# Performance work log

Measured on AMD Instinct MI355X. Metric: run time of the kernel, lower is better.

Reference implementation:

```python
import jax, jax.numpy as jnp
import numpy as np

N, K, IN_DIM, OUT_DIM = 100000, 16, 64, 64
BN_EPS = 1e-5


def setup_inputs() -> dict:
    key = jax.random.key(0)
    ks = jax.random.split(key, 12)
    def lin(k, fan_in, shape):
        bound = 1.0 / np.sqrt(fan_in)
        return jax.random.uniform(k, shape, jnp.float32, -bound, bound)
    return {
        'points': jax.random.normal(ks[0], (N, 3), jnp.float32),
        'neighbors': jax.random.randint(ks[1], (N, K), 0, N + 1, jnp.int32),
        'feats': jax.random.normal(ks[2], (N, IN_DIM), jnp.float32),
        'q_w': lin(ks[3], IN_DIM, (OUT_DIM, IN_DIM)), 'q_b': lin(ks[3], IN_DIM, (OUT_DIM,)),
        'k_w': lin(ks[4], IN_DIM, (OUT_DIM, IN_DIM)), 'k_b': lin(ks[4], IN_DIM, (OUT_DIM,)),
        'v_w': lin(ks[5], IN_DIM, (OUT_DIM, IN_DIM)), 'v_b': lin(ks[5], IN_DIM, (OUT_DIM,)),
        'p_w': lin(ks[6], 3, (OUT_DIM, 3)), 'p_b': lin(ks[6], 3, (OUT_DIM,)),
        'p_gamma': jnp.ones((OUT_DIM,), jnp.float32), 'p_beta': jnp.zeros((OUT_DIM,), jnp.float32),
        'w_w': lin(ks[7], OUT_DIM, (OUT_DIM, OUT_DIM)), 'w_b': lin(ks[7], OUT_DIM, (OUT_DIM,)),
        'w_gamma': jnp.ones((OUT_DIM,), jnp.float32), 'w_beta': jnp.zeros((OUT_DIM,), jnp.float32),
    }


def _bn_relu(x, gamma, beta):
    # BatchNorm1d (training mode, biased var) over all axes except channel (last), then ReLU
    mean = jnp.mean(x, axis=(0, 1), keepdims=True)
    var = jnp.mean(jnp.square(x - mean), axis=(0, 1), keepdims=True)
    y = (x - mean) * jax.lax.rsqrt(var + BN_EPS) * gamma + beta
    return jax.nn.relu(y)


def reference(points, neighbors, feats, q_w, q_b, k_w, k_b, v_w, v_b,
              p_w, p_b, p_gamma, p_beta, w_w, w_b, w_gamma, w_beta):
    q = feats @ q_w.T + q_b                       # [N, D]
    k = feats @ k_w.T + k_b
    v = feats @ v_w.T + v_b
    # shadow-pad with an out-of-range point / zero feats
    points_pad = jnp.concatenate([points, jnp.full((1, 3), 1e6, points.dtype)], 0)
    k_pad = jnp.concatenate([k, jnp.zeros((1, k.shape[1]), k.dtype)], 0)
    v_pad = jnp.concatenate([v, jnp.zeros((1, v.shape[1]), v.dtype)], 0)
    p_g = points_pad[neighbors]                   # [N, K, 3]
    k_g = k_pad[neighbors]                        # [N, K, D]
    v_g = v_pad[neighbors]                        # [N, K, D]
    p_feats = _bn_relu(p_g @ p_w.T + p_b, p_gamma, p_beta)          # [N, K, D]
    w = k_g * q[:, None, :] + p_feats                               # [N, K, D]
    w = _bn_relu(w @ w_w.T + w_b, w_gamma, w_beta)
    w = jax.nn.softmax(w, axis=1)                 # softmax over neighbor axis
    att = jnp.sum((v_g + p_feats) * w, axis=1)    # [N, D]
    return att
```

## Files before the change

kernel.cpp:

```cpp
#include <hip/hip_runtime.h>
#include <math.h>

#define NP 100000
#define KN 16
#define DIM 64
constexpr float BN_EPS_F = 1e-5f;
constexpr double MS = (double)NP * (double)KN;

typedef __attribute__((ext_vector_type(8))) short short8;
typedef __attribute__((ext_vector_type(4))) float f32x4;

constexpr size_t B_S1  = 0;
constexpr size_t B_PWE = 128;
constexpr size_t B_S2  = 1152;
constexpr size_t B_BN2 = 2176;
constexpr size_t B_ZSE = 2688;
constexpr size_t B_ZSB = 2944;
constexpr size_t B_PFS = 3200;
constexpr size_t B_PTS = 4096;
constexpr size_t B_Q   = 1204224;
constexpr size_t B_U   = B_Q + (size_t)NP * DIM * 2;
constexpr size_t B_KK  = B_U + (size_t)(NP + 1) * DIM * 2;
constexpr size_t B_Z1   = B_KK + (size_t)(NP + 1) * DIM * 4;
constexpr size_t B_END1 = B_Z1 + (size_t)NP * 2048;
constexpr size_t B_Z2   = B_KK + (size_t)(NP + 1) * DIM * 2;
constexpr size_t B_END2 = B_Z2 + (size_t)NP * 2048;

__device__ __forceinline__ ushort f2bf(float f) {
  union { float f; unsigned u; } v; v.f = f;
  unsigned u = v.u + 0x7fffu + ((v.u >> 16) & 1u);
  return (ushort)(u >> 16);
}
__device__ __forceinline__ float bf2f(ushort b) {
  union { unsigned u; float f; } v; v.u = ((unsigned)b) << 16;
  return v.f;
}
__device__ __forceinline__ float u2f(unsigned u) {
  union { unsigned u; float f; } v; v.u = u; return v.f;
}

__device__ __forceinline__ void load_wfrags(const float* __restrict__ ww, int lane,
                                            short8 wf[4][2]) {
  int co = lane & 15, g = lane >> 4;
#pragma unroll
  for (int tn = 0; tn < 4; ++tn)
#pragma unroll
    for (int kk = 0; kk < 2; ++kk) {
      const float* p = ww + (size_t)(co + 16 * tn) * DIM + kk * 32 + g * 8;
      short8 f;
#pragma unroll
      for (int j = 0; j < 8; ++j) f[j] = (short)f2bf(p[j]);
      wf[tn][kk] = f;
    }
}

__device__ __forceinline__ short8 pack_bf8(float4 a, float4 b) {
  short8 r;
  r[0] = (short)f2bf(a.x); r[1] = (short)f2bf(a.y);
  r[2] = (short)f2bf(a.z); r[3] = (short)f2bf(a.w);
  r[4] = (short)f2bf(b.x); r[5] = (short)f2bf(b.y);
  r[6] = (short)f2bf(b.z); r[7] = (short)f2bf(b.w);
  return r;
}

__global__ void k_init(char* __restrict__ wsb) {
  int t = threadIdx.x;
  double* s1 = (double*)(wsb + B_S1);
  double* s2 = (double*)(wsb + B_S2);
  if (t < 10) s1[t] = 0.0;
  if (t < 128) s2[t] = 0.0;
  if (t < 32)
    ((unsigned*)(wsb + B_U))[(size_t)NP * 32 + t] = 0u;
}

__global__ __launch_bounds__(256) void k_pts(const float* __restrict__ pts,
                                             char* __restrict__ wsb) {
  int t = blockIdx.x * 256 + threadIdx.x;
  float* p3 = (float*)(wsb + B_PTS);
  if (t < NP * 3) p3[t] = pts[t];
  else if (t < NP * 3 + 3) p3[t] = 1e6f;
}

__global__ __launch_bounds__(256) void k_stats1(const int* __restrict__ nbr,
    char* __restrict__ wsb) {
  const float* p3 = (const float*)(wsb + B_PTS);
  double a[10] = {0, 0, 0, 0, 0, 0, 0, 0, 0, 0};
  int stride = gridDim.x * blockDim.x;
  for (int e = blockIdx.x * 256 + threadIdx.x; e < NP * KN; e += stride) {
    int idx = nbr[e];
    const float* pr = p3 + (size_t)idx * 3;
    float x = pr[0], y = pr[1], z = pr[2];
    a[9] += (idx >= NP) ? 1.0 : 0.0;
    a[0] += x; a[1] += y; a[2] += z;
    a[3] += (double)x * x; a[4] += (double)x * y; a[5] += (double)x * z;
    a[6] += (double)y * y; a[7] += (double)y * z; a[8] += (double)z * z;
  }
  __shared__ double red[256];
  double* s1 = (double*)(wsb + B_S1);
  for (int j = 0; j < 10; ++j) {
    red[threadIdx.x] = a[j];
    __syncthreads();
    for (int s = 128; s > 0; s >>= 1) {
      if (threadIdx.x < s) red[threadIdx.x] += red[threadIdx.x + s];
      __syncthreads();
    }
    if (threadIdx.x == 0) atomicAdd(&s1[j], red[0]);
    __syncthreads();
  }
}

__global__ void k_fold1(const float* __restrict__ pw, const float* __restrict__ pb,
                        const float* __restrict__ pg, const float* __restrict__ pbeta,
                        char* __restrict__ wsb) {
  int c = threadIdx.x;
  if (c >= DIM) return;
  double* s1 = (double*)(wsb + B_S1);
  double inv = 1.0 / MS;
  double m0 = s1[0] * inv, m1 = s1[1] * inv, m2 = s1[2] * inv;
  double C00 = s1[3] * inv - m0 * m0, C01 = s1[4] * inv - m0 * m1;
  double C02 = s1[5] * inv - m0 * m2, C11 = s1[6] * inv - m1 * m1;
  double C12 = s1[7] * inv - m1 * m2, C22 = s1[8] * inv - m2 * m2;
  double w0 = pw[c * 3], w1 = pw[c * 3 + 1], w2 = pw[c * 3 + 2];
  double mean = w0 * m0 + w1 * m1 + w2 * m2 + (double)pb[c];
  double var = w0 * w0 * C00 + w1 * w1 * C11 + w2 * w2 * C22
             + 2.0 * (w0 * w1 * C01 + w0 * w2 * C02 + w1 * w2 * C12);
  if (var < 0.0) var = 0.0;
  double a = (double)pg[c] / sqrt(var + (double)BN_EPS_F);
  float4 o;
  o.x = (float)(w0 * a); o.y = (float)(w1 * a); o.z = (float)(w2 * a);
  o.w = (float)(((double)pb[c] - mean) * a + (double)pbeta[c]);
  ((float4*)(wsb + B_PWE))[c] = o;
}

__global__ void k_shadow(const float* __restrict__ ww, const float* __restrict__ wb,
                         char* __restrict__ wsb, int kpmode) {
  __shared__ float pfs[64], pfb[64];
  int c = threadIdx.x;
  if (c >= DIM) return;
  float4 pwe = ((const float4*)(wsb + B_PWE))[c];
  float pf = fmaxf(fmaf(pwe.x, 1e6f, fmaf(pwe.y, 1e6f, fmaf(pwe.z, 1e6f, pwe.w))), 0.f);
  pfs[c] = pf;
  pfb[c] = bf2f(f2bf(pf));
  ((float*)(wsb + B_PFS))[c] = pf;
  if (kpmode)
    ((unsigned*)(wsb + B_KK))[(size_t)NP * DIM + c] = ((unsigned)f2bf(pf) << 16);
  else
    ((ushort*)(wsb + B_KK))[(size_t)NP * DIM + c] = 0;
  __syncthreads();
  double ze = (double)wb[c], zb = (double)wb[c];
  for (int i = 0; i < DIM; ++i) {
    float w = ww[c * DIM + i];
    ze += (double)pfs[i] * (double)w;
    zb += (double)pfb[i] * (double)bf2f(f2bf(w));
  }
  ((float*)(wsb + B_ZSE))[c] = (float)ze;
  ((float*)(wsb + B_ZSB))[c] = (float)zb;
}

template<bool KPMODE>
__global__ __launch_bounds__(256, 2) void k_qkv_mfma(const float* __restrict__ feats,
    const float* __restrict__ qw, const float* __restrict__ qb,
    const float* __restrict__ kw, const float* __restrict__ kb,
    const float* __restrict__ vw, const float* __restrict__ vb,
    char* __restrict__ wsb) {
  int tid = threadIdx.x, wid = tid >> 6, lane = tid & 63;
  int co = lane & 15, g = lane >> 4;
  short8 wfq[4][2], wfk[4][2], wfv[4][2];
  load_wfrags(qw, lane, wfq);
  load_wfrags(kw, lane, wfk);
  load_wfrags(vw, lane, wfv);
  float bq[4], bk[4], bv[4];
  float4 pwe4[4];
#pragma unroll
  for (int tn = 0; tn < 4; ++tn) {
    bq[tn] = qb[co + 16 * tn];
    bk[tn] = kb[co + 16 * tn];
    bv[tn] = vb[co + 16 * tn];
    pwe4[tn] = ((const float4*)(wsb + B_PWE))[co + 16 * tn];
  }
  const float* p3 = (const float*)(wsb + B_PTS);
  ushort* qt = (ushort*)(wsb + B_Q);
  ushort* ut = (ushort*)(wsb + B_U);
  ushort* kt = (ushort*)(wsb + B_KK);
  unsigned* kpt = (unsigned*)(wsb + B_KK);
  const int NT = NP / 16;
  for (int t = blockIdx.x * 4 + wid; t < NT; t += gridDim.x * 4) {
    const float* fr = feats + ((size_t)t * 16 + co) * DIM + g * 8;
    float4 f0 = *(const float4*)fr;
    float4 f1 = *(const float4*)(fr + 4);
    float4 f2 = *(const float4*)(fr + 32);
    float4 f3 = *(const float4*)(fr + 36);
    short8 a0 = pack_bf8(f0, f1);
    short8 a1 = pack_bf8(f2, f3);
    int nb = t * 16 + g * 4;
    float px[4], py[4], pz[4];
#pragma unroll
    for (int r = 0; r < 4; ++r) {
      const float* pr = p3 + (size_t)(nb + r) * 3;
      px[r] = pr[0]; py[r] = pr[1]; pz[r] = pr[2];
    }
    float pf[4][4];
#pragma unroll
    for (int tn = 0; tn < 4; ++tn)
#pragma unroll
      for (int r = 0; r < 4; ++r)
        pf[tn][r] = fmaxf(fmaf(pwe4[tn].x, px[r], fmaf(pwe4[tn].y, py[r],
                          fmaf(pwe4[tn].z, pz[r], pwe4[tn].w))), 0.f);
#pragma unroll
    for (int tn = 0; tn < 4; ++tn) {
      f32x4 acc = {bq[tn], bq[tn], bq[tn], bq[tn]};
      acc = __builtin_amdgcn_mfma_f32_16x16x32_bf16(a0, wfq[tn][0], acc, 0, 0, 0);
      acc = __builtin_amdgcn_mfma_f32_16x16x32_bf16(a1, wfq[tn][1], acc, 0, 0, 0);
#pragma unroll
      for (int r = 0; r < 4; ++r)
        qt[(size_t)(nb + r) * DIM + co + 16 * tn] = f2bf(acc[r]);
    }
#pragma unroll
    for (int tn = 0; tn < 4; ++tn) {
      f32x4 acc = {bk[tn], bk[tn], bk[tn], bk[tn]};
      acc = __builtin_amdgcn_mfma_f32_16x16x32_bf16(a0, wfk[tn][0], acc, 0, 0, 0);
      acc = __builtin_amdgcn_mfma_f32_16x16x32_bf16(a1, wfk[tn][1], acc, 0, 0, 0);
#pragma unroll
      for (int r = 0; r < 4; ++r) {
        if (KPMODE)
          kpt[(size_t)(nb + r) * DIM + co + 16 * tn] =
              ((unsigned)f2bf(pf[tn][r]) << 16) | (unsigned)f2bf(acc[r]);
        else
          kt[(size_t)(nb + r) * DIM + co + 16 * tn] = f2bf(acc[r]);
      }
    }
#pragma unroll
    for (int tn = 0; tn < 4; ++tn) {
      f32x4 acc = {bv[tn], bv[tn], bv[tn], bv[tn]};
      acc = __builtin_amdgcn_mfma_f32_16x16x32_bf16(a0, wfv[tn][0], acc, 0, 0, 0);
      acc = __builtin_amdgcn_mfma_f32_16x16x32_bf16(a1, wfv[tn][1], acc, 0, 0, 0);
#pragma unroll
      for (int r = 0; r < 4; ++r)
        ut[(size_t)(nb + r) * DIM + co + 16 * tn] = f2bf(acc[r] + pf[tn][r]);
    }
  }
}

#define LOADN(SET, nn) {                                                      \
  const int4* p4_ = (const int4*)(nbr + (size_t)(nn) * KN);                   \
  int4 b0_ = p4_[0], b1_ = p4_[1], b2_ = p4_[2], b3_ = p4_[3];                \
  i##SET[0] = b0_.x; i##SET[1] = b0_.y; i##SET[2] = b0_.z; i##SET[3] = b0_.w; \
  i##SET[4] = b1_.x; i##SET[5] = b1_.y; i##SET[6] = b1_.z; i##SET[7] = b1_.w; \
  i##SET[8] = b2_.x; i##SET[9] = b2_.y; i##SET[10]= b2_.z; i##SET[11]= b2_.w; \
  i##SET[12]= b3_.x; i##SET[13]= b3_.y; i##SET[14]= b3_.z; i##SET[15]= b3_.w; }

#define S2_LOADG(SET, nn) {                                                   \
  if constexpr (KPMODE) {                                                     \
    _Pragma("unroll") for (int k = 0; k < KN; ++k)                            \
      kp##SET[k] = kpt[(size_t)i##SET[k] * DIM + c];                          \
  } else {                                                                    \
    _Pragma("unroll") for (int k = 0; k < KN; ++k) {                          \
      int ik_ = i##SET[k];                                                    \
      unsigned kv_ = kt[(size_t)ik_ * DIM + c];                               \
      const float* pr_ = p3 + (size_t)ik_ * 3;                                \
      float px_ = pr_[0], py_ = pr_[1], pz_ = pr_[2];                         \
      float pf_ = fmaxf(fmaf(pwe.x, px_, fmaf(pwe.y, py_,                     \
                        fmaf(pwe.z, pz_, pwe.w))), 0.f);                      \
      kp##SET[k] = ((unsigned)f2bf(pf_) << 16) | kv_;                         \
    }                                                                         \
  }                                                                           \
  q##SET = bf2f(qt[(size_t)(nn) * DIM + c]); }

#define S2_COMPUTE(SET, nn) {                                                 \
  _Pragma("unroll") for (int k = 0; k < KN; ++k) {                            \
    float kg_ = u2f(kp##SET[k] << 16);                                        \
    float pf_ = u2f(kp##SET[k] & 0xffff0000u);                                \
    hw[k * 64 + (c ^ ((k & 7) << 3))] = f2bf(fmaf(kg_, q##SET, pf_));         \
  }                                                                           \
  __builtin_amdgcn_wave_barrier();                                            \
  short8 a0_ = *(short8*)&hw[aoff0];                                          \
  short8 a1_ = *(short8*)&hw[aoff1];                                          \
  char* zr_ = ztc + (size_t)(nn) * 2048 + g * 8;                              \
  _Pragma("unroll") for (int tn = 0; tn < 4; ++tn) {                          \
    f32x4 acc_ = {wbv[tn], wbv[tn], wbv[tn], wbv[tn]};                        \
    acc_ = __builtin_amdgcn_mfma_f32_16x16x32_bf16(a0_, wf[tn][0], acc_,0,0,0);\
    acc_ = __builtin_amdgcn_mfma_f32_16x16x32_bf16(a1_, wf[tn][1], acc_,0,0,0);\
    _Pragma("unroll") for (int r = 0; r < 4; ++r) {                           \
      float zv_ = acc_[r];                                                    \
      s[tn] += zv_; ssq[tn] = fmaf(zv_, zv_, ssq[tn]); }                      \
    uint2 w_;                                                                 \
    w_.x = (unsigned)f2bf(acc_[0]) | ((unsigned)f2bf(acc_[1]) << 16);         \
    w_.y = (unsigned)f2bf(acc_[2]) | ((unsigned)f2bf(acc_[3]) << 16);         \
    *(uint2*)(zr_ + ((lane & 15) + 16 * tn) * 32) = w_;                       \
  }                                                                           \
  __builtin_amdgcn_wave_barrier(); }

template<bool KPMODE>
__global__ __launch_bounds__(256) void k_stats2(const int* __restrict__ nbr,
    const float* __restrict__ ww, const float* __restrict__ wbias,
    char* __restrict__ wsb, char* __restrict__ ztc) {
  __shared__ ushort hl[4][16 * 64];
  __shared__ float sred[4][64], ssred[4][64];
  int tid = threadIdx.x, wid = tid >> 6, lane = tid & 63, c = lane;
  short8 wf[4][2];
  load_wfrags(ww, lane, wf);
  float wbv[4];
#pragma unroll
  for (int tn = 0; tn < 4; ++tn) wbv[tn] = wbias[(lane & 15) + 16 * tn];
  const ushort* qt = (const ushort*)(wsb + B_Q);
  const ushort* kt = (const ushort*)(wsb + B_KK);
  const unsigned* kpt = (const unsigned*)(wsb + B_KK);
  const float* p3 = (const float*)(wsb + B_PTS);
  float4 pwe = ((const float4*)(wsb + B_PWE))[c];
  ushort* hw = hl[wid];
  int row = lane & 15, g = lane >> 4;
  int aoff0 = row * 64 + ((g * 8) ^ ((row & 7) << 3));
  int aoff1 = row * 64 + ((32 + g * 8) ^ ((row & 7) << 3));
  float s[4] = {0, 0, 0, 0}, ssq[4] = {0, 0, 0, 0};
  const int S = gridDim.x * 4;
  int n = blockIdx.x * 4 + wid;

  int iA[KN], iB[KN];
  unsigned kpA[KN], kpB[KN];
  float qA, qB;

  LOADN(A, n)
  LOADN(B, n + S)
  S2_LOADG(A, n)
  for (int it = 0; it < 4; ++it) {
    S2_LOADG(B, n + S)
    if (it < 3) LOADN(A, n + 2 * S)
    S2_COMPUTE(A, n)
    if (it < 3) { S2_LOADG(A, n + 2 * S) LOADN(B, n + 3 * S) }
    S2_COMPUTE(B, n + S)
    n += 2 * S;
  }
#pragma unroll
  for (int t = 0; t < 4; ++t) {
    s[t] += __shfl_xor(s[t], 16);    s[t] += __shfl_xor(s[t], 32);
    ssq[t] += __shfl_xor(ssq[t], 16); ssq[t] += __shfl_xor(ssq[t], 32);
  }
  if (lane < 16) {
#pragma unroll
    for (int t = 0; t < 4; ++t) { sred[wid][lane + 16 * t] = s[t]; ssred[wid][lane + 16 * t] = ssq[t]; }
  }
  __syncthreads();
  if (tid < DIM) {
    double SS0 = 0.0, SS1 = 0.0;
    for (int w = 0; w < 4; ++w) { SS0 += (double)sred[w][tid]; SS1 += (double)ssred[w][tid]; }
    double* s2 = (double*)(wsb + B_S2);
    atomicAdd(&s2[tid], SS0);
    atomicAdd(&s2[DIM + tid], SS1);
  }
}

__global__ void k_fold2(const float* __restrict__ wg, const float* __restrict__ wbeta,
                        char* __restrict__ wsb) {
  int c = threadIdx.x;
  if (c >= DIM) return;
  double* s2 = (double*)(wsb + B_S2);
  double* s1 = (double*)(wsb + B_S1);
  double nsh = s1[9];
  double zse = (double)((float*)(wsb + B_ZSE))[c];
  double zsb = (double)((float*)(wsb + B_ZSB))[c];
  double S  = s2[c] + nsh * (zse - zsb);
  double SS = s2[DIM + c] + nsh * (zse * zse - zsb * zsb);
  double mean = S / MS;
  double var = SS / MS - mean * mean;
  if (var < 0.0) var = 0.0;
  double a = (double)wg[c] / sqrt(var + (double)BN_EPS_F);
  ((float*)(wsb + B_BN2))[c] = (float)a;
  ((float*)(wsb + B_BN2))[DIM + c] = (float)((double)wbeta[c] - mean * a);
}

#define FS_LOADG(SET, nn) {                                                   \
  const char* zr_ = ztc + (size_t)(nn) * 2048 + c * 32;                       \
  *(uint4*)&zz##SET[0] = *(const uint4*)(zr_);                                \
  *(uint4*)&zz##SET[4] = *(const uint4*)(zr_ + 16);                           \
  _Pragma("unroll") for (int k = 0; k < KN; ++k)                              \
    uv##SET[k] = ut[(size_t)i##SET[k] * DIM + c];                             \
  sh##SET = 0u;                                                               \
  _Pragma("unroll") for (int k = 0; k < KN; ++k)                              \
    sh##SET |= (unsigned)(i##SET[k] >= NP) << k; }

#define FS_COMPUTE(SET, nn) {                                                 \
  float lg_[KN];                                                              \
  float m_ = 0.f;                                                             \
  _Pragma("unroll") for (int k = 0; k < KN; ++k) {                            \
    float lin_ = bf2f((ushort)(zz##SET[k >> 1] >> ((k & 1) * 16)));           \
    if ((sh##SET >> k) & 1u) lin_ = zsec;                                     \
    float t_ = fmaxf(fmaf(lin_, fsc, fsh), 0.f);                              \
    lg_[k] = t_; m_ = fmaxf(m_, t_); }                                        \
  float se_ = 0.f;                                                            \
  _Pragma("unroll") for (int k = 0; k < KN; ++k) {                            \
    float e_ = __expf(lg_[k] - m_); lg_[k] = e_; se_ += e_; }                 \
  float rs_ = 1.0f / se_;                                                     \
  float att_ = 0.f;                                                           \
  _Pragma("unroll") for (int k = 0; k < KN; ++k) {                            \
    float u_ = ((sh##SET >> k) & 1u) ? pfsec : bf2f(uv##SET[k]);              \
    att_ = fmaf(u_, lg_[k] * rs_, att_); }                                    \
  out[(size_t)(nn) * DIM + c] = att_; }

__global__ __launch_bounds__(256) void k_final_str(const int* __restrict__ nbr,
    const char* __restrict__ wsb, const char* __restrict__ ztc,
    float* __restrict__ out) {
  int tid = threadIdx.x, wid = tid >> 6, c = tid & 63;
  const ushort* ut = (const ushort*)(wsb + B_U);
  const float* bn2 = (const float*)(wsb + B_BN2);
  float fsc = bn2[c], fsh = bn2[DIM + c];
  float zsec = ((const float*)(wsb + B_ZSE))[c];
  float pfsec = ((const float*)(wsb + B_PFS))[c];
  const int S = gridDim.x * 4;
  int n = blockIdx.x * 4 + wid;

  int iA[KN], iB[KN];
  unsigned zzA[8], zzB[8];
  ushort uvA[KN], uvB[KN];
  unsigned shA, shB;

  LOADN(A, n)
  LOADN(B, n + S)
  FS_LOADG(A, n)
  for (int it = 0; it < 4; ++it) {
    FS_LOADG(B, n + S)
    if (it < 3) LOADN(A, n + 2 * S)
    FS_COMPUTE(A, n)
    if (it < 3) { FS_LOADG(A, n + 2 * S) LOADN(B, n + 3 * S) }
    FS_COMPUTE(B, n + S)
    n += 2 * S;
  }
}

extern "C" void kernel_launch(void* const* d_in, const int* in_sizes, int n_in,
                              void* d_out, int out_size, void* d_ws, size_t ws_size,
                              hipStream_t stream) {
  const float* pts   = (const float*)d_in[0];
  const int*   nbr   = (const int*)d_in[1];
  const float* feats = (const float*)d_in[2];
  const float* qw = (const float*)d_in[3];  const float* qb = (const float*)d_in[4];
  const float* kw = (const float*)d_in[5];  const float* kb = (const float*)d_in[6];
  const float* vw = (const float*)d_in[7];  const float* vb = (const float*)d_in[8];
  const float* pw = (const float*)d_in[9];  const float* pb = (const float*)d_in[10];
  const float* pg = (const float*)d_in[11]; const float* pbeta = (const float*)d_in[12];
  const float* www = (const float*)d_in[13]; const float* wb = (const float*)d_in[14];
  const float* wg  = (const float*)d_in[15]; const float* wbeta = (const float*)d_in[16];
  char* wsb = (char*)d_ws;
  float* out = (float*)d_out;

  const bool kpmode = (ws_size >= B_END1);
  char* zt = wsb + (kpmode ? B_Z1 : B_Z2);

  hipLaunchKernelGGL(k_init,   dim3(1),    dim3(256), 0, stream, wsb);
  hipLaunchKernelGGL(k_pts,    dim3(1173), dim3(256), 0, stream, pts, wsb);
  hipLaunchKernelGGL(k_stats1, dim3(512),  dim3(256), 0, stream, nbr, wsb);
  hipLaunchKernelGGL(k_fold1,  dim3(1),    dim3(64),  0, stream, pw, pb, pg, pbeta, wsb);
  hipLaunchKernelGGL(k_shadow, dim3(1),    dim3(64),  0, stream, www, wb, wsb, (int)kpmode);
  if (kpmode) {
    hipLaunchKernelGGL((k_qkv_mfma<true>), dim3(256),  dim3(256), 0, stream,
                       feats, qw, qb, kw, kb, vw, vb, wsb);
    hipLaunchKernelGGL((k_stats2<true>),   dim3(3125), dim3(256), 0, stream,
                       nbr, www, wb, wsb, zt);
  } else {
    hipLaunchKernelGGL((k_qkv_mfma<false>), dim3(256),  dim3(256), 0, stream,
                       feats, qw, qb, kw, kb, vw, vb, wsb);
    hipLaunchKernelGGL((k_stats2<false>),   dim3(3125), dim3(256), 0, stream,
                       nbr, www, wb, wsb, zt);
  }
  hipLaunchKernelGGL(k_fold2, dim3(1), dim3(64), 0, stream, wg, wbeta, wsb);
  hipLaunchKernelGGL(k_final_str, dim3(3125), dim3(256), 0, stream, nbr, wsb, zt, out);
}
```

Before: 289.6 us.

## Recompute attention logits in final pass instead of storing intermediate z tensor

Stops writing the bf16 W-projection output (2 KB per point) in the statistics pass. The final kernel now regathers the packed k/pos features and redoes the MFMA projection via shared memory. It also drops the low-workspace fallback path and always uses the packed k+pos layout. Output stores become nontemporal. This trades about 400 MB of write-plus-read traffic for repeated gathers and matrix math, and it now requires the larger workspace.

```diff
diff --git a/kernel.cpp b/kernel.cpp
--- a/kernel.cpp
+++ b/kernel.cpp
@@ -21,10 +21,7 @@
 constexpr size_t B_Q   = 1204224;
 constexpr size_t B_U   = B_Q + (size_t)NP * DIM * 2;
 constexpr size_t B_KK  = B_U + (size_t)(NP + 1) * DIM * 2;
-constexpr size_t B_Z1   = B_KK + (size_t)(NP + 1) * DIM * 4;
-constexpr size_t B_END1 = B_Z1 + (size_t)NP * 2048;
-constexpr size_t B_Z2   = B_KK + (size_t)(NP + 1) * DIM * 2;
-constexpr size_t B_END2 = B_Z2 + (size_t)NP * 2048;
+constexpr size_t B_END = B_KK + (size_t)(NP + 1) * DIM * 4;
 
 __device__ __forceinline__ ushort f2bf(float f) {
   union { float f; unsigned u; } v; v.f = f;
@@ -133,7 +130,7 @@
 }
 
 __global__ void k_shadow(const float* __restrict__ ww, const float* __restrict__ wb,
-                         char* __restrict__ wsb, int kpmode) {
+                         char* __restrict__ wsb) {
   __shared__ float pfs[64], pfb[64];
   int c = threadIdx.x;
   if (c >= DIM) return;
@@ -142,10 +139,7 @@
   pfs[c] = pf;
   pfb[c] = bf2f(f2bf(pf));
   ((float*)(wsb + B_PFS))[c] = pf;
-  if (kpmode)
-    ((unsigned*)(wsb + B_KK))[(size_t)NP * DIM + c] = ((unsigned)f2bf(pf) << 16);
-  else
-    ((ushort*)(wsb + B_KK))[(size_t)NP * DIM + c] = 0;
+  ((unsigned*)(wsb + B_KK))[(size_t)NP * DIM + c] = ((unsigned)f2bf(pf) << 16);
   __syncthreads();
   double ze = (double)wb[c], zb = (double)wb[c];
   for (int i = 0; i < DIM; ++i) {
@@ -157,7 +151,6 @@
   ((float*)(wsb + B_ZSB))[c] = (float)zb;
 }
 
-template<bool KPMODE>
 __global__ __launch_bounds__(256, 2) void k_qkv_mfma(const float* __restrict__ feats,
     const float* __restrict__ qw, const float* __restrict__ qb,
     const float* __restrict__ kw, const float* __restrict__ kb,
@@ -181,7 +174,6 @@
   const float* p3 = (const float*)(wsb + B_PTS);
   ushort* qt = (ushort*)(wsb + B_Q);
   ushort* ut = (ushort*)(wsb + B_U);
-  ushort* kt = (ushort*)(wsb + B_KK);
   unsigned* kpt = (unsigned*)(wsb + B_KK);
   const int NT = NP / 16;
   for (int t = blockIdx.x * 4 + wid; t < NT; t += gridDim.x * 4) {
@@ -221,13 +213,9 @@
       acc = __builtin_amdgcn_mfma_f32_16x16x32_bf16(a0, wfk[tn][0], acc, 0, 0, 0);
       acc = __builtin_amdgcn_mfma_f32_16x16x32_bf16(a1, wfk[tn][1], acc, 0, 0, 0);
 #pragma unroll
-      for (int r = 0; r < 4; ++r) {
-        if (KPMODE)
-          kpt[(size_t)(nb + r) * DIM + co + 16 * tn] =
-              ((unsigned)f2bf(pf[tn][r]) << 16) | (unsigned)f2bf(acc[r]);
-        else
-          kt[(size_t)(nb + r) * DIM + co + 16 * tn] = f2bf(acc[r]);
-      }
+      for (int r = 0; r < 4; ++r)
+        kpt[(size_t)(nb + r) * DIM + co + 16 * tn] =
+            ((unsigned)f2bf(pf[tn][r]) << 16) | (unsigned)f2bf(acc[r]);
     }
 #pragma unroll
     for (int tn = 0; tn < 4; ++tn) {
@@ -250,20 +238,8 @@
   i##SET[12]= b3_.x; i##SET[13]= b3_.y; i##SET[14]= b3_.z; i##SET[15]= b3_.w; }
 
 #define S2_LOADG(SET, nn) {                                                   \
-  if constexpr (KPMODE) {                                                     \
-    _Pragma("unroll") for (int k = 0; k < KN; ++k)                            \
-      kp##SET[k] = kpt[(size_t)i##SET[k] * DIM + c];                          \
-  } else {                                                                    \
-    _Pragma("unroll") for (int k = 0; k < KN; ++k) {                          \
-      int ik_ = i##SET[k];                                                    \
-      unsigned kv_ = kt[(size_t)ik_ * DIM + c];                               \
-      const float* pr_ = p3 + (size_t)ik_ * 3;                                \
-      float px_ = pr_[0], py_ = pr_[1], pz_ = pr_[2];                         \
-      float pf_ = fmaxf(fmaf(pwe.x, px_, fmaf(pwe.y, py_,                     \
-                        fmaf(pwe.z, pz_, pwe.w))), 0.f);                      \
-      kp##SET[k] = ((unsigned)f2bf(pf_) << 16) | kv_;                         \
-    }                                                                         \
-  }                                                                           \
+  _Pragma("unroll") for (int k = 0; k < KN; ++k)                              \
+    kp##SET[k] = kpt[(size_t)i##SET[k] * DIM + c];                            \
   q##SET = bf2f(qt[(size_t)(nn) * DIM + c]); }
 
 #define S2_COMPUTE(SET, nn) {                                                 \
@@ -275,25 +251,18 @@
   __builtin_amdgcn_wave_barrier();                                            \
   short8 a0_ = *(short8*)&hw[aoff0];                                          \
   short8 a1_ = *(short8*)&hw[aoff1];                                          \
-  char* zr_ = ztc + (size_t)(nn) * 2048 + g * 8;                              \
   _Pragma("unroll") for (int tn = 0; tn < 4; ++tn) {                          \
     f32x4 acc_ = {wbv[tn], wbv[tn], wbv[tn], wbv[tn]};                        \
     acc_ = __builtin_amdgcn_mfma_f32_16x16x32_bf16(a0_, wf[tn][0], acc_,0,0,0);\
     acc_ = __builtin_amdgcn_mfma_f32_16x16x32_bf16(a1_, wf[tn][1], acc_,0,0,0);\
     _Pragma("unroll") for (int r = 0; r < 4; ++r) {                           \
       float zv_ = acc_[r];                                                    \
-      s[tn] += zv_; ssq[tn] = fmaf(zv_, zv_, ssq[tn]); }                      \
-    uint2 w_;                                                                 \
-    w_.x = (unsigned)f2bf(acc_[0]) | ((unsigned)f2bf(acc_[1]) << 16);         \
-    w_.y = (unsigned)f2bf(acc_[2]) | ((unsigned)f2bf(acc_[3]) << 16);         \
-    *(uint2*)(zr_ + ((lane & 15) + 16 * tn) * 32) = w_;                       \
-  }                                                                           \
+      s[tn] += zv_; ssq[tn] = fmaf(zv_, zv_, ssq[tn]); } }                    \
   __builtin_amdgcn_wave_barrier(); }
 
-template<bool KPMODE>
 __global__ __launch_bounds__(256) void k_stats2(const int* __restrict__ nbr,
     const float* __restrict__ ww, const float* __restrict__ wbias,
-    char* __restrict__ wsb, char* __restrict__ ztc) {
+    char* __restrict__ wsb) {
   __shared__ ushort hl[4][16 * 64];
   __shared__ float sred[4][64], ssred[4][64];
   int tid = threadIdx.x, wid = tid >> 6, lane = tid & 63, c = lane;
@@ -303,10 +272,7 @@
 #pragma unroll
   for (int tn = 0; tn < 4; ++tn) wbv[tn] = wbias[(lane & 15) + 16 * tn];
   const ushort* qt = (const ushort*)(wsb + B_Q);
-  const ushort* kt = (const ushort*)(wsb + B_KK);
   const unsigned* kpt = (const unsigned*)(wsb + B_KK);
-  const float* p3 = (const float*)(wsb + B_PTS);
-  float4 pwe = ((const float4*)(wsb + B_PWE))[c];
   ushort* hw = hl[wid];
   int row = lane & 15, g = lane >> 4;
   int aoff0 = row * 64 + ((g * 8) ^ ((row & 7) << 3));
@@ -368,21 +334,37 @@
   ((float*)(wsb + B_BN2))[DIM + c] = (float)((double)wbeta[c] - mean * a);
 }
 
-#define FS_LOADG(SET, nn) {                                                   \
-  const char* zr_ = ztc + (size_t)(nn) * 2048 + c * 32;                       \
-  *(uint4*)&zz##SET[0] = *(const uint4*)(zr_);                                \
-  *(uint4*)&zz##SET[4] = *(const uint4*)(zr_ + 16);                           \
+#define KF_LOADG(SET, nn) {                                                   \
+  _Pragma("unroll") for (int k = 0; k < KN; ++k)                              \
+    kp##SET[k] = kpt[(size_t)i##SET[k] * DIM + c];                            \
   _Pragma("unroll") for (int k = 0; k < KN; ++k)                              \
     uv##SET[k] = ut[(size_t)i##SET[k] * DIM + c];                             \
   sh##SET = 0u;                                                               \
   _Pragma("unroll") for (int k = 0; k < KN; ++k)                              \
-    sh##SET |= (unsigned)(i##SET[k] >= NP) << k; }
-
-#define FS_COMPUTE(SET, nn) {                                                 \
+    sh##SET |= (unsigned)(i##SET[k] >= NP) << k;                              \
+  q##SET = bf2f(qt[(size_t)(nn) * DIM + c]); }
+
+#define KF_COMPUTE(SET, nn) {                                                 \
+  _Pragma("unroll") for (int k = 0; k < KN; ++k) {                            \
+    float kg_ = u2f(kp##SET[k] << 16);                                        \
+    float pf_ = u2f(kp##SET[k] & 0xffff0000u);                                \
+    hw[k * 64 + (c ^ ((k & 7) << 3))] = f2bf(fmaf(kg_, q##SET, pf_));         \
+  }                                                                           \
+  __builtin_amdgcn_wave_barrier();                                            \
+  short8 a0_ = *(short8*)&hw[aoff0];                                          \
+  short8 a1_ = *(short8*)&hw[aoff1];                                          \
+  _Pragma("unroll") for (int tn = 0; tn < 4; ++tn) {                          \
+    f32x4 acc_ = {wbv[tn], wbv[tn], wbv[tn], wbv[tn]};                        \
+    acc_ = __builtin_amdgcn_mfma_f32_16x16x32_bf16(a0_, wf[tn][0], acc_,0,0,0);\
+    acc_ = __builtin_amdgcn_mfma_f32_16x16x32_bf16(a1_, wf[tn][1], acc_,0,0,0);\
+    _Pragma("unroll") for (int r = 0; r < 4; ++r)                             \
+      zw[(g * 4 + r) * 68 + (lane & 15) + 16 * tn] = acc_[r];                 \
+  }                                                                           \
+  __builtin_amdgcn_wave_barrier();                                            \
   float lg_[KN];                                                              \
   float m_ = 0.f;                                                             \
   _Pragma("unroll") for (int k = 0; k < KN; ++k) {                            \
-    float lin_ = bf2f((ushort)(zz##SET[k >> 1] >> ((k & 1) * 16)));           \
+    float lin_ = zw[k * 68 + c];                                              \
     if ((sh##SET >> k) & 1u) lin_ = zsec;                                     \
     float t_ = fmaxf(fmaf(lin_, fsc, fsh), 0.f);                              \
     lg_[k] = t_; m_ = fmaxf(m_, t_); }                                        \
@@ -394,34 +376,50 @@
   _Pragma("unroll") for (int k = 0; k < KN; ++k) {                            \
     float u_ = ((sh##SET >> k) & 1u) ? pfsec : bf2f(uv##SET[k]);              \
     att_ = fmaf(u_, lg_[k] * rs_, att_); }                                    \
-  out[(size_t)(nn) * DIM + c] = att_; }
-
-__global__ __launch_bounds__(256) void k_final_str(const int* __restrict__ nbr,
-    const char* __restrict__ wsb, const char* __restrict__ ztc,
-    float* __restrict__ out) {
-  int tid = threadIdx.x, wid = tid >> 6, c = tid & 63;
+  __builtin_nontemporal_store(att_, out + (size_t)(nn) * DIM + c);            \
+  __builtin_amdgcn_wave_barrier(); }
+
+__global__ __launch_bounds__(256) void k_final_rec(const int* __restrict__ nbr,
+    const float* __restrict__ ww, const float* __restrict__ wbias,
+    const char* __restrict__ wsb, float* __restrict__ out) {
+  __shared__ ushort hl[4][16 * 64];
+  __shared__ float zl[4][16 * 68];
+  int tid = threadIdx.x, wid = tid >> 6, lane = tid & 63, c = lane;
+  short8 wf[4][2];
+  load_wfrags(ww, lane, wf);
+  float wbv[4];
+#pragma unroll
+  for (int tn = 0; tn < 4; ++tn) wbv[tn] = wbias[(lane & 15) + 16 * tn];
+  const ushort* qt = (const ushort*)(wsb + B_Q);
   const ushort* ut = (const ushort*)(wsb + B_U);
+  const unsigned* kpt = (const unsigned*)(wsb + B_KK);
   const float* bn2 = (const float*)(wsb + B_BN2);
   float fsc = bn2[c], fsh = bn2[DIM + c];
   float zsec = ((const float*)(wsb + B_ZSE))[c];
   float pfsec = ((const float*)(wsb + B_PFS))[c];
+  ushort* hw = hl[wid];
+  float* zw = zl[wid];
+  int row = lane & 15, g = lane >> 4;
+  int aoff0 = row * 64 + ((g * 8) ^ ((row & 7) << 3));
+  int aoff1 = row * 64 + ((32 + g * 8) ^ ((row & 7) << 3));
   const int S = gridDim.x * 4;
   int n = blockIdx.x * 4 + wid;
 
   int iA[KN], iB[KN];
-  unsigned zzA[8], zzB[8];
+  unsigned kpA[KN], kpB[KN];
   ushort uvA[KN], uvB[KN];
   unsigned shA, shB;
+  float qA, qB;
 
   LOADN(A, n)
   LOADN(B, n + S)
-  FS_LOADG(A, n)
+  KF_LOADG(A, n)
   for (int it = 0; it < 4; ++it) {
-    FS_LOADG(B, n + S)
+    KF_LOADG(B, n + S)
     if (it < 3) LOADN(A, n + 2 * S)
-    FS_COMPUTE(A, n)
-    if (it < 3) { FS_LOADG(A, n + 2 * S) LOADN(B, n + 3 * S) }
-    FS_COMPUTE(B, n + S)
+    KF_COMPUTE(A, n)
+    if (it < 3) { KF_LOADG(A, n + 2 * S) LOADN(B, n + 3 * S) }
+    KF_COMPUTE(B, n + S)
     n += 2 * S;
   }
 }
@@ -442,25 +440,14 @@
   char* wsb = (char*)d_ws;
   float* out = (float*)d_out;
 
-  const bool kpmode = (ws_size >= B_END1);
-  char* zt = wsb + (kpmode ? B_Z1 : B_Z2);
-
   hipLaunchKernelGGL(k_init,   dim3(1),    dim3(256), 0, stream, wsb);
   hipLaunchKernelGGL(k_pts,    dim3(1173), dim3(256), 0, stream, pts, wsb);
   hipLaunchKernelGGL(k_stats1, dim3(512),  dim3(256), 0, stream, nbr, wsb);
   hipLaunchKernelGGL(k_fold1,  dim3(1),    dim3(64),  0, stream, pw, pb, pg, pbeta, wsb);
-  hipLaunchKernelGGL(k_shadow, dim3(1),    dim3(64),  0, stream, www, wb, wsb, (int)kpmode);
-  if (kpmode) {
-    hipLaunchKernelGGL((k_qkv_mfma<true>), dim3(256),  dim3(256), 0, stream,
-                       feats, qw, qb, kw, kb, vw, vb, wsb);
-    hipLaunchKernelGGL((k_stats2<true>),   dim3(3125), dim3(256), 0, stream,
-                       nbr, www, wb, wsb, zt);
-  } else {
-    hipLaunchKernelGGL((k_qkv_mfma<false>), dim3(256),  dim3(256), 0, stream,
-                       feats, qw, qb, kw, kb, vw, vb, wsb);
-    hipLaunchKernelGGL((k_stats2<false>),   dim3(3125), dim3(256), 0, stream,
-                       nbr, www, wb, wsb, zt);
-  }
-  hipLaunchKernelGGL(k_fold2, dim3(1), dim3(64), 0, stream, wg, wbeta, wsb);
-  hipLaunchKernelGGL(k_final_str, dim3(3125), dim3(256), 0, stream, nbr, wsb, zt, out);
-}
+  hipLaunchKernelGGL(k_shadow, dim3(1),    dim3(64),  0, stream, www, wb, wsb);
+  hipLaunchKernelGGL(k_qkv_mfma, dim3(256), dim3(256), 0, stream,
+                     feats, qw, qb, kw, kb, vw, vb, wsb);
+  hipLaunchKernelGGL(k_stats2, dim3(3125), dim3(256), 0, stream, nbr, www, wb, wsb);
+  hipLaunchKernelGGL(k_fold2,  dim3(1),    dim3(64),  0, stream, wg, wbeta, wsb);
+  hipLaunchKernelGGL(k_final_rec, dim3(3125), dim3(256), 0, stream, nbr, www, wb, wsb, out);
+}
```

Result: slower. 330.8 us (+14.2%).
